# Kernel tuning notes

Hardware: AMD Instinct MI355X
Metric: run time of the kernel (lower is better)

## Reference

```python
import jax, jax.numpy as jnp
import numpy as np

BN_EPS = 1e-5
STRIDE = 4
K_NEAREST = 16


def _fps(xyz, m):
    """Farthest point sampling. xyz: [n,3] -> indices [m] (seeded at point 0)."""
    n = xyz.shape[0]

    def body(i, state):
        dist, idxs, last = state
        d = jnp.sum((xyz - xyz[last]) ** 2, axis=-1)
        dist = jnp.minimum(dist, d)
        nxt = jnp.argmax(dist).astype(jnp.int32)
        return dist, idxs.at[i].set(nxt), nxt

    init = (jnp.full((n,), 1e10, xyz.dtype), jnp.zeros((m,), jnp.int32), jnp.int32(0))
    _, idxs, _ = jax.lax.fori_loop(1, m, body, init)
    return idxs


def _knn(q, x, k):
    """q: [m,3] queries, x: [n,3] points -> [m,k] nearest-neighbor indices."""
    d = jnp.sum((q[:, None, :] - x[None, :, :]) ** 2, axis=-1)  # [m,n]
    _, idx = jax.lax.top_k(-d, k)
    return idx


def setup_inputs() -> dict:
    key = jax.random.key(0)
    k0, k1, k2 = jax.random.split(key, 3)
    B, N, IN_CH, OUT_CH = 4, 8192, 64, 128
    events = jax.random.uniform(k0, (B, N, 4), dtype=jnp.float32)  # xyz in [0,1) + time
    features = jax.random.normal(k1, (B, N, IN_CH), dtype=jnp.float32)
    W = jax.random.normal(k2, (4 + IN_CH, OUT_CH), dtype=jnp.float32) / np.float32(np.sqrt(4 + IN_CH))
    b = jnp.zeros((OUT_CH,), jnp.float32)
    gamma = jnp.ones((OUT_CH,), jnp.float32)
    beta = jnp.zeros((OUT_CH,), jnp.float32)
    return dict(events=events, features=features, W=W, b=b, gamma=gamma, beta=beta)


def reference(events, features, W, b, gamma, beta):
    B, N, _ = events.shape
    m = N // STRIDE  # down_offsets = offsets // stride with equal-size samples
    xyz = events[..., :3]
    xyz_c = jax.lax.stop_gradient(xyz)  # indices are non-differentiable

    # farthest point sampling per cloud -> [B, m]
    down_idx = jax.vmap(lambda p: _fps(p, m))(xyz_c)
    down_xyz = jnp.take_along_axis(xyz_c, down_idx[..., None], axis=1)  # [B,m,3]
    # k nearest neighbors of each sampled point -> [B, m, K]
    idx = jax.vmap(lambda q, x: _knn(q, x, K_NEAREST))(down_xyz, xyz_c)

    down_events = jnp.take_along_axis(events, down_idx[..., None], axis=1)  # [B,m,4]
    grouped_events = jax.vmap(lambda e, i: e[i])(events, idx)               # [B,m,K,4]
    grouped_events_norm = grouped_events - down_events[:, :, None, :]
    grouped_features = jax.vmap(lambda f, i: f[i])(features, idx)           # [B,m,K,in_ch]
    g = jnp.concatenate([grouped_events_norm, grouped_features], axis=-1)   # [B,m,K,4+in_ch]

    # Linear -> BatchNorm1d (training batch stats over all points & neighbors) -> ReLU
    h = jnp.einsum('bmkc,cd->bmkd', g, W) + b
    mu = jnp.mean(h, axis=(0, 1, 2))
    var = jnp.var(h, axis=(0, 1, 2))
    h = (h - mu) * jax.lax.rsqrt(var + BN_EPS) * gamma + beta
    h = jax.nn.relu(h)

    down_features = jnp.max(h, axis=2)  # max-pool over K neighbors -> [B,m,out_ch]
    return down_events, down_features
```

## Files before the change

### kernel.cpp

```cpp
#include <hip/hip_runtime.h>

#define N_PTS 8192
#define M_PTS 2048
#define K_NN 16
#define IN_CH 64
#define G_CH 68
#define OUT_CH 128
#define KCAP 128

__device__ __forceinline__ float subrn(float a, float b) {
    float r; asm("v_sub_f32 %0, %1, %2" : "=v"(r) : "v"(a), "v"(b)); return r;
}
__device__ __forceinline__ float mulrn(float a, float b) {
    float r; asm("v_mul_f32 %0, %1, %2" : "=v"(r) : "v"(a), "v"(b)); return r;
}
__device__ __forceinline__ float addrn(float a, float b) {
    float r; asm("v_add_f32 %0, %1, %2" : "=v"(r) : "v"(a), "v"(b)); return r;
}
__device__ __forceinline__ float sqdist_rn(float ax, float ay, float az,
                                           float bx, float by, float bz) {
    float dx = subrn(ax, bx);
    float dy = subrn(ay, by);
    float dz = subrn(az, bz);
    return addrn(addrn(mulrn(dx, dx), mulrn(dy, dy)), mulrn(dz, dz));
}

typedef float v2f __attribute__((ext_vector_type(2)));
__device__ __forceinline__ v2f pk_add(v2f a, v2f b) {
    v2f r; asm("v_pk_add_f32 %0, %1, %2" : "=v"(r) : "v"(a), "v"(b)); return r;
}
__device__ __forceinline__ v2f pk_mul(v2f a, v2f b) {
    v2f r; asm("v_pk_mul_f32 %0, %1, %2" : "=v"(r) : "v"(a), "v"(b)); return r;
}

template <int CTRL, int RM>
__device__ __forceinline__ float dppmaxf(float x) {
    int r = __builtin_amdgcn_update_dpp(0, __float_as_int(x), CTRL, RM, 0xf, false);
    return fmaxf(x, __int_as_float(r));
}
template <int CTRL, int RM>
__device__ __forceinline__ int dppmini(int x) {
    int r = __builtin_amdgcn_update_dpp(0x7fffffff, x, CTRL, RM, 0xf, false);
    return min(x, r);
}
__device__ __forceinline__ float wave_max64(float x) {
    x = dppmaxf<0xB1, 0xf>(x);
    x = dppmaxf<0x4E, 0xf>(x);
    x = dppmaxf<0x141, 0xf>(x);
    x = dppmaxf<0x140, 0xf>(x);
    x = dppmaxf<0x142, 0xa>(x);
    x = dppmaxf<0x143, 0xc>(x);
    return x;
}
__device__ __forceinline__ int wave_min64(int x) {
    x = dppmini<0xB1, 0xf>(x);
    x = dppmini<0x4E, 0xf>(x);
    x = dppmini<0x141, 0xf>(x);
    x = dppmini<0x140, 0xf>(x);
    x = dppmini<0x142, 0xa>(x);
    x = dppmini<0x143, 0xc>(x);
    return x;
}
__device__ __forceinline__ float row16_max(float x) {
    x = dppmaxf<0xB1, 0xf>(x);
    x = dppmaxf<0x4E, 0xf>(x);
    x = dppmaxf<0x141, 0xf>(x);
    x = dppmaxf<0x140, 0xf>(x);
    return x;
}
__device__ __forceinline__ int row16_min(int x) {
    x = dppmini<0xB1, 0xf>(x);
    x = dppmini<0x4E, 0xf>(x);
    x = dppmini<0x141, 0xf>(x);
    x = dppmini<0x140, 0xf>(x);
    return x;
}
__device__ __forceinline__ float group8_max(float x) {
    x = dppmaxf<0xB1, 0xf>(x);
    x = dppmaxf<0x4E, 0xf>(x);
    x = dppmaxf<0x141, 0xf>(x);
    return x;
}

__global__ __launch_bounds__(1024) void fps_kernel(const float4* __restrict__ events4,
                                                   int* __restrict__ down_idx,
                                                   float4* __restrict__ out_de) {
    extern __shared__ char smem[];
    float*  rv  = (float*)smem;
    int*    ri  = (int*)(smem + 64);
    int*    ssel= (int*)(smem + 128);
    float4* spt = (float4*)(smem + 128 + 4 * M_PTS);

    const int b = blockIdx.x;
    const int tid = threadIdx.x;
    const float4* ev = events4 + (size_t)b * N_PTS;

    for (int i = tid; i < N_PTS; i += 1024) spt[i] = ev[i];
    if (tid == 0) { ssel[0] = 0; down_idx[b * M_PTS] = 0; }
    __syncthreads();

    v2f px[4], py[4], pz[4];
    float dist[8];
#pragma unroll
    for (int pp = 0; pp < 4; ++pp) {
        float4 f0 = spt[(2 * pp) * 1024 + tid];
        float4 f1 = spt[(2 * pp + 1) * 1024 + tid];
        px[pp] = (v2f){f0.x, f1.x};
        py[pp] = (v2f){f0.y, f1.y};
        pz[pp] = (v2f){f0.z, f1.z};
        dist[2 * pp] = 1e10f; dist[2 * pp + 1] = 1e10f;
    }

    int last = 0;
    const int wave = tid >> 6;
    const int lane = tid & 63;

    for (int i = 1; i < M_PTS; ++i) {
        float4 L = spt[last];
        const float nlx = -L.x, nly = -L.y, nlz = -L.z;
        const v2f nx2 = (v2f){nlx, nlx};
        const v2f ny2 = (v2f){nly, nly};
        const v2f nz2 = (v2f){nlz, nlz};
        float bd = -1.0f;
#pragma unroll
        for (int pp = 0; pp < 4; ++pp) {
            v2f dx = pk_add(px[pp], nx2);
            v2f dy = pk_add(py[pp], ny2);
            v2f dz = pk_add(pz[pp], nz2);
            v2f s  = pk_add(pk_add(pk_mul(dx, dx), pk_mul(dy, dy)), pk_mul(dz, dz));
            float d0 = fminf(dist[2 * pp],     s.x);
            float d1 = fminf(dist[2 * pp + 1], s.y);
            dist[2 * pp] = d0; dist[2 * pp + 1] = d1;
            bd = fmaxf(bd, d0); bd = fmaxf(bd, d1);
        }
        int bi = 0;
#pragma unroll
        for (int j = 7; j >= 0; --j) if (dist[j] == bd) bi = j * 1024 + tid;

        float wm = wave_max64(bd);
        if (lane == 63) rv[wave] = wm;
        __syncthreads();
        float bm = row16_max(rv[lane & 15]);
        int cand = (bd == bm) ? bi : 0x7fffffff;
        int wmin = wave_min64(cand);
        if (lane == 63) ri[wave] = wmin;
        __syncthreads();
        int winner = row16_min(ri[lane & 15]);
        if (tid == 0) {
            ssel[i] = winner;
            down_idx[b * M_PTS + i] = winner;
        }
        last = winner;
    }
    __syncthreads();

    for (int i = tid; i < M_PTS; i += 1024) {
        out_de[(size_t)b * M_PTS + i] = spt[ssel[i]];
    }
}

__global__ __launch_bounds__(256) void knn_kernel(const float4* __restrict__ events4,
                                                  const int* __restrict__ down_idx,
                                                  int* __restrict__ knn_idx) {
    extern __shared__ char smem[];
    float* sx   = (float*)smem;
    float* sy   = sx + N_PTS;
    float* sz   = sy + N_PTS;
    float* cd   = sz + N_PTS;
    int*   ci   = (int*)(cd + 32 * KCAP);
    int*   scnt = (int*)(ci + 32 * KCAP);

    const int b    = blockIdx.x >> 6;
    const int qg   = blockIdx.x & 63;
    const int tid  = threadIdx.x;
    const int ql   = tid >> 3;
    const int part = tid & 7;

    const float4* ev = events4 + (size_t)b * N_PTS;
    for (int i = tid; i < N_PTS; i += 256) {
        float4 e = ev[i];
        sx[i] = e.x; sy[i] = e.y; sz[i] = e.z;
    }
    if (tid < 32) scnt[tid] = 0;
    __syncthreads();

    const int q  = qg * 32 + ql;
    const int qi = down_idx[b * M_PTS + q];
    const float qx = sx[qi], qy = sy[qi], qz = sz[qi];

    float m1 = 1e30f, m2 = 1e30f;
    for (int i = 0; i < N_PTS / 8; ++i) {
        const int p = i * 8 + part;
        float d = sqdist_rn(sx[p], sy[p], sz[p], qx, qy, qz);
        float lo = fminf(m1, d);
        m2 = fminf(m2, fmaxf(m1, d));
        m1 = lo;
    }
    const float T = group8_max(m2);

    for (int i = 0; i < N_PTS / 8; ++i) {
        const int p = i * 8 + part;
        float d = sqdist_rn(sx[p], sy[p], sz[p], qx, qy, qz);
        if (d <= T) {
            int pos = atomicAdd(&scnt[ql], 1);
            if (pos < KCAP) { cd[ql * KCAP + pos] = d; ci[ql * KCAP + pos] = p; }
        }
    }
    __syncthreads();

    if (part == 0) {
        float nd[16]; int ni[16];
#pragma unroll
        for (int j = 0; j < 16; ++j) { nd[j] = 1e30f; ni[j] = 0x7fffffff; }
        float wmax = 1e30f; int widx = 0x7fffffff; int wslot = 0;
        const int n = scnt[ql];
        const int lim = (n <= KCAP) ? n : 0;
        for (int t = 0; t < lim; ++t) {
            float d = cd[ql * KCAP + t];
            int   p = ci[ql * KCAP + t];
            if (d < wmax || (d == wmax && p < widx)) {
#pragma unroll
                for (int j = 0; j < 16; ++j) if (j == wslot) { nd[j] = d; ni[j] = p; }
                float m_ = -1.0f; int mix_ = -1; int ms_ = 0;
#pragma unroll
                for (int j = 0; j < 16; ++j)
                    if (nd[j] > m_ || (nd[j] == m_ && ni[j] > mix_)) { m_ = nd[j]; mix_ = ni[j]; ms_ = j; }
                wmax = m_; widx = mix_; wslot = ms_;
            }
        }
        if (n > KCAP) {
            for (int p = 0; p < N_PTS; ++p) {
                float d = sqdist_rn(sx[p], sy[p], sz[p], qx, qy, qz);
                if (d < wmax || (d == wmax && p < widx)) {
#pragma unroll
                    for (int j = 0; j < 16; ++j) if (j == wslot) { nd[j] = d; ni[j] = p; }
                    float m_ = -1.0f; int mix_ = -1; int ms_ = 0;
#pragma unroll
                    for (int j = 0; j < 16; ++j)
                        if (nd[j] > m_ || (nd[j] == m_ && ni[j] > mix_)) { m_ = nd[j]; mix_ = ni[j]; ms_ = j; }
                    wmax = m_; widx = mix_; wslot = ms_;
                }
            }
        }
        int* out = knn_idx + ((size_t)(b * M_PTS + q)) * K_NN;
#pragma unroll
        for (int j = 0; j < 16; ++j) out[j] = ni[j];
    }
}

__global__ __launch_bounds__(256) void gmm_kernel(const float* __restrict__ events,
                                                  const float* __restrict__ features,
                                                  const float* __restrict__ W,
                                                  const float* __restrict__ bias,
                                                  const int* __restrict__ knn_idx,
                                                  const float* __restrict__ de,
                                                  float* __restrict__ hmax_g,
                                                  float* __restrict__ hmin_g,
                                                  float* __restrict__ gsum,
                                                  float* __restrict__ gsq) {
    __shared__ __align__(16) float sg[16 * G_CH];
    __shared__ float scomb[2 * OUT_CH];

    const int b   = blockIdx.x >> 7;
    const int qg  = blockIdx.x & 127;
    const int tid = threadIdx.x;
    const int d   = tid & 127;
    const int kh  = tid >> 7;

    float w[G_CH];
#pragma unroll
    for (int c = 0; c < G_CH; ++c) w[c] = W[c * OUT_CH + d];
    const float breg = bias[d];

    float ssum = 0.f, ssq = 0.f;
    const float4* sg4 = (const float4*)sg;

    for (int qq = 0; qq < 16; ++qq) {
        const int q = qg * 16 + qq;
        const int base = b * M_PTS + q;
        for (int j = tid; j < 16 * G_CH; j += 256) {
            int k = j / G_CH;
            int c = j - k * G_CH;
            int nb = knn_idx[base * K_NN + k];
            float v;
            if (c < 4) v = events[((size_t)(b * N_PTS + nb)) * 4 + c] - de[(size_t)base * 4 + c];
            else       v = features[((size_t)(b * N_PTS + nb)) * IN_CH + (c - 4)];
            sg[j] = v;
        }
        __syncthreads();

        float hmax = -1e30f, hmin = 1e30f;
#pragma unroll
        for (int k2 = 0; k2 < 8; ++k2) {
            const int k = kh * 8 + k2;
            float acc = breg;
#pragma unroll
            for (int c4 = 0; c4 < 17; ++c4) {
                float4 g = sg4[k * 17 + c4];
                acc = fmaf(g.x, w[4 * c4 + 0], acc);
                acc = fmaf(g.y, w[4 * c4 + 1], acc);
                acc = fmaf(g.z, w[4 * c4 + 2], acc);
                acc = fmaf(g.w, w[4 * c4 + 3], acc);
            }
            hmax = fmaxf(hmax, acc);
            hmin = fminf(hmin, acc);
            ssum += acc;
            ssq = fmaf(acc, acc, ssq);
        }
        if (kh == 1) { scomb[d] = hmax; scomb[OUT_CH + d] = hmin; }
        __syncthreads();
        if (kh == 0) {
            hmax = fmaxf(hmax, scomb[d]);
            hmin = fminf(hmin, scomb[OUT_CH + d]);
            hmax_g[(size_t)base * OUT_CH + d] = hmax;
            hmin_g[(size_t)base * OUT_CH + d] = hmin;
        }
        __syncthreads();
    }
    if (kh == 1) { scomb[d] = ssum; scomb[OUT_CH + d] = ssq; }
    __syncthreads();
    if (kh == 0) {
        atomicAdd(&gsum[d], ssum + scomb[d]);
        atomicAdd(&gsq[d],  ssq  + scomb[OUT_CH + d]);
    }
}

__global__ __launch_bounds__(256) void fin_kernel(const float* __restrict__ hmax_g,
                                                  const float* __restrict__ hmin_g,
                                                  const float* __restrict__ gsum,
                                                  const float* __restrict__ gsq,
                                                  const float* __restrict__ gamma,
                                                  const float* __restrict__ beta,
                                                  float* __restrict__ out) {
    const size_t e = (size_t)blockIdx.x * 256 + threadIdx.x;
    const int d = (int)(e & 127);
    const float inv_cnt = 1.0f / 131072.0f;
    float mu  = gsum[d] * inv_cnt;
    float var = gsq[d] * inv_cnt - mu * mu;
    float a   = gamma[d] * rsqrtf(var + 1e-5f);
    float sh  = fmaf(-mu, a, beta[d]);
    float hv  = (a >= 0.f) ? hmax_g[e] : hmin_g[e];
    float r   = fmaf(a, hv, sh);
    out[32768 + e] = r > 0.f ? r : 0.f;
}

extern "C" void kernel_launch(void* const* d_in, const int* in_sizes, int n_in,
                              void* d_out, int out_size, void* d_ws, size_t ws_size,
                              hipStream_t stream) {
    const float* events   = (const float*)d_in[0];
    const float* features = (const float*)d_in[1];
    const float* W        = (const float*)d_in[2];
    const float* bias     = (const float*)d_in[3];
    const float* gamma    = (const float*)d_in[4];
    const float* beta     = (const float*)d_in[5];
    float* out = (float*)d_out;
    char* ws = (char*)d_ws;

    int*   down_idx = (int*)ws;
    int*   knn_idx  = (int*)(ws + 32768);
    float* gsum     = (float*)(ws + 32768 + 524288);
    float* gsq      = gsum + OUT_CH;
    float* hmaxg    = (float*)(ws + 558080);
    float* hming    = hmaxg + (size_t)4 * M_PTS * OUT_CH;

    (void)hipMemsetAsync(gsum, 0, 2 * OUT_CH * sizeof(float), stream);

    const size_t fps_lds = 128 + 4 * M_PTS + (size_t)N_PTS * sizeof(float4);
    fps_kernel<<<4, 1024, fps_lds, stream>>>((const float4*)events, down_idx, (float4*)out);

    const size_t knn_lds = (size_t)3 * N_PTS * sizeof(float)
                         + (size_t)32 * KCAP * 8 + 128;
    knn_kernel<<<256, 256, knn_lds, stream>>>((const float4*)events, down_idx, knn_idx);

    gmm_kernel<<<512, 256, 0, stream>>>(events, features, W, bias, knn_idx, out,
                                        hmaxg, hming, gsum, gsq);

    fin_kernel<<<4096, 256, 0, stream>>>(hmaxg, hming, gsum, gsq, gamma, beta, out);
}
```

Before: 2.730 ms.

## Restructure FPS argmax with 512 threads, ballot tie-break, and single barrier reduction

The farthest point sampling kernel now runs 512 threads, each owning 16 contiguous points instead of 8 strided ones. The argmax reduction drops the second block-wide min-reduction pass: a wave ballot picks the lowest candidate lane, which writes its index to shared memory, and the eight wave slots are min-reduced. DPP reductions use mov_dpp with bound_ctrl, and down_idx writes move out of the serial loop into the final copy. The goal is to shorten the per-iteration critical path of the 2047-step serial loop, at the cost of more per-thread work and register use.

```diff
diff --git a/kernel.cpp b/kernel.cpp
--- a/kernel.cpp
+++ b/kernel.cpp
@@ -33,78 +33,67 @@
     v2f r; asm("v_pk_mul_f32 %0, %1, %2" : "=v"(r) : "v"(a), "v"(b)); return r;
 }
 
+template <int CTRL>
+__device__ __forceinline__ float movdpp_f(float x) {
+    int r = __builtin_amdgcn_mov_dpp(__float_as_int(x), CTRL, 0xf, 0xf, true);
+    return __int_as_float(r);
+}
+template <int CTRL>
+__device__ __forceinline__ int movdpp_i(int x) {
+    return __builtin_amdgcn_mov_dpp(x, CTRL, 0xf, 0xf, true);
+}
 template <int CTRL, int RM>
-__device__ __forceinline__ float dppmaxf(float x) {
+__device__ __forceinline__ float dppmaxf_m(float x) {
     int r = __builtin_amdgcn_update_dpp(0, __float_as_int(x), CTRL, RM, 0xf, false);
     return fmaxf(x, __int_as_float(r));
 }
-template <int CTRL, int RM>
-__device__ __forceinline__ int dppmini(int x) {
-    int r = __builtin_amdgcn_update_dpp(0x7fffffff, x, CTRL, RM, 0xf, false);
-    return min(x, r);
-}
 __device__ __forceinline__ float wave_max64(float x) {
-    x = dppmaxf<0xB1, 0xf>(x);
-    x = dppmaxf<0x4E, 0xf>(x);
-    x = dppmaxf<0x141, 0xf>(x);
-    x = dppmaxf<0x140, 0xf>(x);
-    x = dppmaxf<0x142, 0xa>(x);
-    x = dppmaxf<0x143, 0xc>(x);
+    x = fmaxf(x, movdpp_f<0xB1>(x));
+    x = fmaxf(x, movdpp_f<0x4E>(x));
+    x = fmaxf(x, movdpp_f<0x141>(x));
+    x = fmaxf(x, movdpp_f<0x140>(x));
+    x = dppmaxf_m<0x142, 0xa>(x);
+    x = dppmaxf_m<0x143, 0xc>(x);
     return x;
 }
-__device__ __forceinline__ int wave_min64(int x) {
-    x = dppmini<0xB1, 0xf>(x);
-    x = dppmini<0x4E, 0xf>(x);
-    x = dppmini<0x141, 0xf>(x);
-    x = dppmini<0x140, 0xf>(x);
-    x = dppmini<0x142, 0xa>(x);
-    x = dppmini<0x143, 0xc>(x);
+__device__ __forceinline__ float group8_max(float x) {
+    x = fmaxf(x, movdpp_f<0xB1>(x));
+    x = fmaxf(x, movdpp_f<0x4E>(x));
+    x = fmaxf(x, movdpp_f<0x141>(x));
     return x;
 }
-__device__ __forceinline__ float row16_max(float x) {
-    x = dppmaxf<0xB1, 0xf>(x);
-    x = dppmaxf<0x4E, 0xf>(x);
-    x = dppmaxf<0x141, 0xf>(x);
-    x = dppmaxf<0x140, 0xf>(x);
+__device__ __forceinline__ int group8_min_i(int x) {
+    x = min(x, movdpp_i<0xB1>(x));
+    x = min(x, movdpp_i<0x4E>(x));
+    x = min(x, movdpp_i<0x141>(x));
     return x;
 }
-__device__ __forceinline__ int row16_min(int x) {
-    x = dppmini<0xB1, 0xf>(x);
-    x = dppmini<0x4E, 0xf>(x);
-    x = dppmini<0x141, 0xf>(x);
-    x = dppmini<0x140, 0xf>(x);
-    return x;
-}
-__device__ __forceinline__ float group8_max(float x) {
-    x = dppmaxf<0xB1, 0xf>(x);
-    x = dppmaxf<0x4E, 0xf>(x);
-    x = dppmaxf<0x141, 0xf>(x);
-    return x;
-}
-
-__global__ __launch_bounds__(1024) void fps_kernel(const float4* __restrict__ events4,
-                                                   int* __restrict__ down_idx,
-                                                   float4* __restrict__ out_de) {
+
+__global__ __launch_bounds__(512) void fps_kernel(const float4* __restrict__ events4,
+                                                  int* __restrict__ down_idx,
+                                                  float4* __restrict__ out_de) {
     extern __shared__ char smem[];
-    float*  rv  = (float*)smem;
-    int*    ri  = (int*)(smem + 64);
-    int*    ssel= (int*)(smem + 128);
-    float4* spt = (float4*)(smem + 128 + 4 * M_PTS);
+    float*  rv   = (float*)smem;
+    int*    wsl  = (int*)(smem + 32);
+    int*    ssel = (int*)(smem + 64);
+    float4* spt  = (float4*)(smem + 64 + 4 * M_PTS);
 
     const int b = blockIdx.x;
     const int tid = threadIdx.x;
+    const int wave = tid >> 6;
+    const int lane = tid & 63;
     const float4* ev = events4 + (size_t)b * N_PTS;
 
-    for (int i = tid; i < N_PTS; i += 1024) spt[i] = ev[i];
-    if (tid == 0) { ssel[0] = 0; down_idx[b * M_PTS] = 0; }
-    __syncthreads();
-
-    v2f px[4], py[4], pz[4];
-    float dist[8];
-#pragma unroll
-    for (int pp = 0; pp < 4; ++pp) {
-        float4 f0 = spt[(2 * pp) * 1024 + tid];
-        float4 f1 = spt[(2 * pp + 1) * 1024 + tid];
+    for (int i = tid; i < N_PTS; i += 512) spt[i] = ev[i];
+    if (tid == 0) ssel[0] = 0;
+    __syncthreads();
+
+    v2f px[8], py[8], pz[8];
+    float dist[16];
+#pragma unroll
+    for (int pp = 0; pp < 8; ++pp) {
+        float4 f0 = spt[tid * 16 + 2 * pp];
+        float4 f1 = spt[tid * 16 + 2 * pp + 1];
         px[pp] = (v2f){f0.x, f1.x};
         py[pp] = (v2f){f0.y, f1.y};
         pz[pp] = (v2f){f0.z, f1.z};
@@ -112,50 +101,56 @@
     }
 
     int last = 0;
-    const int wave = tid >> 6;
-    const int lane = tid & 63;
-
     for (int i = 1; i < M_PTS; ++i) {
         float4 L = spt[last];
         const float nlx = -L.x, nly = -L.y, nlz = -L.z;
         const v2f nx2 = (v2f){nlx, nlx};
         const v2f ny2 = (v2f){nly, nly};
         const v2f nz2 = (v2f){nlz, nlz};
-        float bd = -1.0f;
-#pragma unroll
-        for (int pp = 0; pp < 4; ++pp) {
+#pragma unroll
+        for (int pp = 0; pp < 8; ++pp) {
             v2f dx = pk_add(px[pp], nx2);
             v2f dy = pk_add(py[pp], ny2);
             v2f dz = pk_add(pz[pp], nz2);
             v2f s  = pk_add(pk_add(pk_mul(dx, dx), pk_mul(dy, dy)), pk_mul(dz, dz));
-            float d0 = fminf(dist[2 * pp],     s.x);
-            float d1 = fminf(dist[2 * pp + 1], s.y);
-            dist[2 * pp] = d0; dist[2 * pp + 1] = d1;
-            bd = fmaxf(bd, d0); bd = fmaxf(bd, d1);
-        }
-        int bi = 0;
-#pragma unroll
-        for (int j = 7; j >= 0; --j) if (dist[j] == bd) bi = j * 1024 + tid;
+            dist[2 * pp]     = fminf(dist[2 * pp],     s.x);
+            dist[2 * pp + 1] = fminf(dist[2 * pp + 1], s.y);
+        }
+        float m0 = fmaxf(dist[0], dist[1]),  m1 = fmaxf(dist[2], dist[3]);
+        float m2 = fmaxf(dist[4], dist[5]),  m3 = fmaxf(dist[6], dist[7]);
+        float m4 = fmaxf(dist[8], dist[9]),  m5 = fmaxf(dist[10], dist[11]);
+        float m6 = fmaxf(dist[12], dist[13]), m7 = fmaxf(dist[14], dist[15]);
+        m0 = fmaxf(m0, m1); m2 = fmaxf(m2, m3); m4 = fmaxf(m4, m5); m6 = fmaxf(m6, m7);
+        float bd = fmaxf(fmaxf(m0, m2), fmaxf(m4, m6));
 
         float wm = wave_max64(bd);
         if (lane == 63) rv[wave] = wm;
         __syncthreads();
-        float bm = row16_max(rv[lane & 15]);
-        int cand = (bd == bm) ? bi : 0x7fffffff;
-        int wmin = wave_min64(cand);
-        if (lane == 63) ri[wave] = wmin;
-        __syncthreads();
-        int winner = row16_min(ri[lane & 15]);
-        if (tid == 0) {
-            ssel[i] = winner;
-            down_idx[b * M_PTS + i] = winner;
-        }
+        float bm = group8_max(rv[lane & 7]);
+
+        bool cand = (bd == bm);
+        unsigned long long mask = __ballot(cand);
+        if (lane == 0) wsl[wave] = 0x7fffffff;
+        if (mask != 0ULL) {
+            int fl = (int)__ffsll((long long)mask) - 1;
+            if (lane == fl) {
+                int jm = 0;
+#pragma unroll
+                for (int j = 15; j >= 0; --j) if (dist[j] == bd) jm = j;
+                wsl[wave] = tid * 16 + jm;
+            }
+        }
+        __syncthreads();
+        int winner = group8_min_i(wsl[lane & 7]);
+        if (tid == 0) ssel[i] = winner;
         last = winner;
     }
     __syncthreads();
 
-    for (int i = tid; i < M_PTS; i += 1024) {
-        out_de[(size_t)b * M_PTS + i] = spt[ssel[i]];
+    for (int i = tid; i < M_PTS; i += 512) {
+        int s = ssel[i];
+        down_idx[b * M_PTS + i] = s;
+        out_de[(size_t)b * M_PTS + i] = spt[s];
     }
 }
 
@@ -365,8 +360,8 @@
 
     (void)hipMemsetAsync(gsum, 0, 2 * OUT_CH * sizeof(float), stream);
 
-    const size_t fps_lds = 128 + 4 * M_PTS + (size_t)N_PTS * sizeof(float4);
-    fps_kernel<<<4, 1024, fps_lds, stream>>>((const float4*)events, down_idx, (float4*)out);
+    const size_t fps_lds = 64 + 4 * M_PTS + (size_t)N_PTS * sizeof(float4);
+    fps_kernel<<<4, 512, fps_lds, stream>>>((const float4*)events, down_idx, (float4*)out);
 
     const size_t knn_lds = (size_t)3 * N_PTS * sizeof(float)
                          + (size_t)32 * KCAP * 8 + 128;
```

Result: faster. 2.443 ms (-10.5%).
